# Kernel optimization log

Hardware: AMD Instinct MI355X
Metric: run time of the kernel (lower is better)

Reference implementation:

```python
import jax, jax.numpy as jnp
import numpy as np

N = 50000
E = 800000
D_IN = 128
D_H = 128
D_OUT = 128
G = 64
EPS = 1e-5


def setup_inputs() -> dict:
    key = jax.random.key(0)
    ks = jax.random.split(key, 16)
    s = 0.05
    x = jax.random.normal(ks[0], (N, D_IN), dtype=jnp.float32)
    edge_index = jax.random.randint(ks[1], (2, E), 0, N, dtype=jnp.int64)
    batch = jnp.sort(jax.random.randint(ks[2], (N,), 0, G, dtype=jnp.int64))
    return {
        "x": x,
        "edge_index": edge_index,
        "batch": batch,
        "W1": jax.random.normal(ks[3], (D_IN, D_H), jnp.float32) * s,
        "a_src1": jax.random.normal(ks[4], (D_H,), jnp.float32) * s,
        "a_dst1": jax.random.normal(ks[5], (D_H,), jnp.float32) * s,
        "b1": jnp.zeros((D_H,), jnp.float32),
        "W2": jax.random.normal(ks[6], (D_H, D_H), jnp.float32) * s,
        "a_src2": jax.random.normal(ks[7], (D_H,), jnp.float32) * s,
        "a_dst2": jax.random.normal(ks[8], (D_H,), jnp.float32) * s,
        "b2": jnp.zeros((D_H,), jnp.float32),
        "ln1_g": jnp.ones((D_H,), jnp.float32),
        "ln1_b": jnp.zeros((D_H,), jnp.float32),
        "ln2_g": jnp.ones((D_H,), jnp.float32),
        "ln2_b": jnp.zeros((D_H,), jnp.float32),
        "fc_W": jax.random.normal(ks[9], (D_H, D_OUT), jnp.float32) * s,
        "fc_b": jnp.zeros((D_OUT,), jnp.float32),
        "bn_g": jnp.ones((D_OUT,), jnp.float32),
        "bn_b": jnp.zeros((D_OUT,), jnp.float32),
    }


def gat_conv(x, src, dst, W, a_src, a_dst, b):
    # PyG GATConv, heads=1, concat=False. src=j (message source), dst=i (target).
    h = x @ W                              # [N, C]
    al_s = h @ a_src                       # [N]
    al_d = h @ a_dst                       # [N]
    alpha = jax.nn.leaky_relu(al_s[src] + al_d[dst], 0.2)  # [E']
    m = jax.ops.segment_max(alpha, dst, num_segments=N)    # segment softmax (stable)
    e = jnp.exp(alpha - m[dst])
    z = jax.ops.segment_sum(e, dst, num_segments=N)
    w = e / z[dst]                          # [E']
    out = jax.ops.segment_sum(w[:, None] * h[src], dst, num_segments=N)
    return out + b


def layer_norm(x, g, b):
    mu = jnp.mean(x, axis=-1, keepdims=True)
    var = jnp.mean((x - mu) ** 2, axis=-1, keepdims=True)
    return (x - mu) * jax.lax.rsqrt(var + EPS) * g + b


def reference(x, edge_index, batch, W1, a_src1, a_dst1, b1, W2, a_src2, a_dst2, b2,
              ln1_g, ln1_b, ln2_g, ln2_b, fc_W, fc_b, bn_g, bn_b):
    # add self loops (PyG GATConv default)
    sl = jnp.arange(N, dtype=edge_index.dtype)
    src = jnp.concatenate([edge_index[0], sl])
    dst = jnp.concatenate([edge_index[1], sl])

    h = jax.nn.relu(gat_conv(x, src, dst, W1, a_src1, a_dst1, b1))
    h = layer_norm(h, ln1_g, ln1_b)
    # dropout is identity in eval
    h = gat_conv(h, src, dst, W2, a_src2, a_dst2, b2)
    h = layer_norm(h, ln2_g, ln2_b)
    h = jax.nn.relu(h)

    # global mean pool over graphs
    sums = jax.ops.segment_sum(h, batch, num_segments=G)            # [G, D_H]
    cnts = jax.ops.segment_sum(jnp.ones((N,), h.dtype), batch, num_segments=G)
    pooled = sums / jnp.maximum(cnts, 1.0)[:, None]

    logits = pooled @ fc_W + fc_b                                   # [G, D_OUT]
    # BatchNorm1d (training-mode batch stats, biased variance)
    mu = jnp.mean(logits, axis=0)
    var = jnp.mean((logits - mu) ** 2, axis=0)
    logits = (logits - mu) * jax.lax.rsqrt(var + EPS) * bn_g + bn_b
    return logits
```

## Files before the change

kernel.cpp:

```cpp
#include <hip/hip_runtime.h>
#include <hip/hip_bf16.h>
#include <math.h>

#define N_NODES 50000
#define N_EDGES 800000
#define EN (N_EDGES + N_NODES)
#define D 128
#define G_GRAPHS 64
#define EPS 1e-5f
#define POOL_ROWS_PER_WAVE 64
#define N_TILES 3125

#define NBUCK 196
#define BCAP 8192
#define EPB 4096
#define BIN_BLOCKS ((EN + EPB - 1) / EPB)

typedef short short8 __attribute__((ext_vector_type(8)));
typedef float f32x4  __attribute__((ext_vector_type(4)));
typedef unsigned short us8 __attribute__((ext_vector_type(8)));

__device__ __forceinline__ float wave_reduce_sum(float v) {
  #pragma unroll
  for (int off = 32; off > 0; off >>= 1) v += __shfl_xor(v, off, 64);
  return v;
}
__device__ __forceinline__ int wave_reduce_sum_i(int v) {
  #pragma unroll
  for (int off = 32; off > 0; off >>= 1) v += __shfl_xor(v, off, 64);
  return v;
}

__device__ __forceinline__ float bf_to_f(unsigned short u) {
  union { unsigned int i; float f; } a;
  a.i = ((unsigned int)u) << 16;
  return a.f;
}
__device__ __forceinline__ unsigned short f_to_bf(float f) {
  union { float f; unsigned int i; } v; v.f = f;
  unsigned int r = v.i + 0x7FFF + ((v.i >> 16) & 1);
  return (unsigned short)(r >> 16);
}


__global__ __launch_bounds__(256) void bin_kernel(
    const int* __restrict__ ei, int* __restrict__ gcnt, uint2* __restrict__ bedges) {
  __shared__ int hist[NBUCK], base[NBUCK], curl[NBUCK];
  int tid = threadIdx.x;
  for (int i = tid; i < NBUCK; i += 256) { hist[i] = 0; curl[i] = 0; }
  __syncthreads();
  int e0 = blockIdx.x * EPB;
  int srcs[16], dsts[16];
  #pragma unroll
  for (int i = 0; i < 16; ++i) {
    int e = e0 + i * 256 + tid;
    int s = -1, d = -1;
    if (e < N_EDGES)   { s = ei[e]; d = ei[N_EDGES + e]; }
    else if (e < EN)   { s = e - N_EDGES; d = s; }
    srcs[i] = s; dsts[i] = d;
    if (d >= 0) atomicAdd(&hist[d >> 8], 1);
  }
  __syncthreads();
  for (int i = tid; i < NBUCK; i += 256)
    base[i] = atomicAdd(&gcnt[i], hist[i]);
  __syncthreads();
  #pragma unroll
  for (int i = 0; i < 16; ++i) {
    int d = dsts[i];
    if (d < 0) continue;
    int b = d >> 8;
    int pos = base[b] + atomicAdd(&curl[b], 1);
    if (pos < BCAP) bedges[(size_t)b * BCAP + pos] = make_uint2((unsigned)srcs[i], (unsigned)d);
  }
}

__global__ __launch_bounds__(256) void bucket_csr_kernel(
    const uint2* __restrict__ bedges, const int* __restrict__ gcnt,
    int* __restrict__ offs, int* __restrict__ esrc, float* __restrict__ sums) {
  __shared__ int hist[256], pex[256], curl[256], scanbuf[256];
  __shared__ int wsum[4];
  int b = blockIdx.x, t = threadIdx.x;
  if (b == 0) {
    for (int i = t; i < G_GRAPHS * D; i += 256) sums[i] = 0.f;
    if (t == 0) offs[N_NODES] = EN;
  }
  int pv = (t < b) ? gcnt[t] : 0;
  int v = wave_reduce_sum_i(pv);
  if ((t & 63) == 0) wsum[t >> 6] = v;
  hist[t] = 0; curl[t] = 0;
  __syncthreads();
  int gb = wsum[0] + wsum[1] + wsum[2] + wsum[3];
  int m = gcnt[b]; if (m > BCAP) m = BCAP;
  int node0 = b << 8;
  const uint2* be = bedges + (size_t)b * BCAP;
  for (int k = t; k < m; k += 256) atomicAdd(&hist[be[k].y & 255], 1);
  __syncthreads();
  int h = hist[t];
  scanbuf[t] = h;
  __syncthreads();
  #pragma unroll
  for (int off = 1; off < 256; off <<= 1) {
    int add = (t >= off) ? scanbuf[t - off] : 0;
    __syncthreads();
    scanbuf[t] += add;
    __syncthreads();
  }
  pex[t] = scanbuf[t] - h;
  int node = node0 + t;
  if (node < N_NODES) offs[node] = gb + pex[t];
  __syncthreads();
  for (int k = t; k < m; k += 256) {
    uint2 e = be[k];
    int n = e.y & 255;
    int r = atomicAdd(&curl[n], 1);
    esrc[gb + pex[n] + r] = (int)e.x;
  }
}


__global__ __launch_bounds__(256) void linear_mfma_kernel(
    const unsigned short* __restrict__ Xb, const float* __restrict__ Xf,
    const float* __restrict__ W,
    const float* __restrict__ a_s, const float* __restrict__ a_d,
    unsigned short* __restrict__ Hb, float* __restrict__ AS, float* __restrict__ AD) {
  __shared__ unsigned short Wl[D * D];
  int tid = threadIdx.x;
  #pragma unroll
  for (int it = 0; it < 64; ++it) {
    int flat = it * 256 + tid;
    int r = flat >> 7, col = flat & 127;
    int c = r >> 5, rem = r & 31, quad = rem >> 3, j = rem & 7;
    int t = col >> 4, l = quad * 16 + (col & 15);
    Wl[((t * 4 + c) * 64 + l) * 8 + j] = f_to_bf(W[flat]);
  }
  int lane = tid & 63, wv = tid >> 6;
  int colI = lane & 15, quad = lane >> 4;
  float as_v[8], ad_v[8];
  #pragma unroll
  for (int t = 0; t < 8; ++t) { as_v[t] = a_s[t * 16 + colI]; ad_v[t] = a_d[t * 16 + colI]; }
  __syncthreads();
  for (int tile = blockIdx.x * 4 + wv; tile < N_TILES; tile += gridDim.x * 4) {
    int row0 = tile * 16;
    short8 afr[4];
    if (Xf) {
      const float* xpf = Xf + (size_t)(row0 + colI) * D + quad * 8;
      #pragma unroll
      for (int c = 0; c < 4; ++c) {
        float4 f0 = *(const float4*)(xpf + c * 32);
        float4 f1 = *(const float4*)(xpf + c * 32 + 4);
        short8 a;
        a[0] = (short)f_to_bf(f0.x); a[1] = (short)f_to_bf(f0.y);
        a[2] = (short)f_to_bf(f0.z); a[3] = (short)f_to_bf(f0.w);
        a[4] = (short)f_to_bf(f1.x); a[5] = (short)f_to_bf(f1.y);
        a[6] = (short)f_to_bf(f1.z); a[7] = (short)f_to_bf(f1.w);
        afr[c] = a;
      }
    } else {
      const unsigned short* xp = Xb + (size_t)(row0 + colI) * D + quad * 8;
      #pragma unroll
      for (int c = 0; c < 4; ++c) afr[c] = *(const short8*)(xp + c * 32);
    }
    f32x4 acc[8];
    #pragma unroll
    for (int t = 0; t < 8; ++t) acc[t] = (f32x4){0.f, 0.f, 0.f, 0.f};
    #pragma unroll
    for (int t = 0; t < 8; ++t) {
      #pragma unroll
      for (int c = 0; c < 4; ++c) {
        short8 bfr = *(const short8*)&Wl[((t * 4 + c) * 64 + lane) * 8];
        acc[t] = __builtin_amdgcn_mfma_f32_16x16x32_bf16(afr[c], bfr, acc[t], 0, 0, 0);
      }
    }
    #pragma unroll
    for (int r = 0; r < 4; ++r) {
      int row = row0 + quad * 4 + r;
      float s = 0.f, dd = 0.f;
      #pragma unroll
      for (int t = 0; t < 8; ++t) {
        float v = acc[t][r];
        Hb[(size_t)row * D + t * 16 + colI] = f_to_bf(v);
        s  = fmaf(v, as_v[t], s);
        dd = fmaf(v, ad_v[t], dd);
      }
      #pragma unroll
      for (int off = 8; off >= 1; off >>= 1) {
        s  += __shfl_xor(s, off, 64);
        dd += __shfl_xor(dd, off, 64);
      }
      if (colI == 0) { AS[row] = s; AD[row] = dd; }
    }
  }
}


__global__ __launch_bounds__(256) void gat_kernel(
    const unsigned short* __restrict__ Hf, const float* __restrict__ AS,
    const float* __restrict__ AD,
    const int* __restrict__ offs, const int* __restrict__ esrc,
    const float* __restrict__ bias, const float* __restrict__ lng, const float* __restrict__ lnb,
    unsigned short* __restrict__ Out, int relu_after) {
  int tid = threadIdx.x;
  int lane = tid & 63;
  int wv = tid >> 6;
  int g4 = lane >> 4, mm = lane & 15;
  int node = blockIdx.x * 16 + wv * 4 + g4;
  if (node >= N_NODES) return;
  int beg = offs[node], end = offs[node + 1];
  float ald = AD[node];
  int base = lane & 48;
  float acc[8];
  #pragma unroll
  for (int d = 0; d < 8; ++d) acc[d] = 0.f;
  float zl = 0.f;
  const unsigned short* hq = Hf + 8 * mm;

  for (int c0 = beg; c0 < end; c0 += 16) {
    int nk = end - c0; if (nk > 16) nk = 16;
    int s_l = 0; float w_l = 0.f;
    if (mm < nk) {
      s_l = esrc[c0 + mm];
      float a = AS[s_l] + ald;
      a = (a > 0.f) ? a : 0.2f * a;
      w_l = __expf(a);
    }
    zl += w_l;
    int   sA = __shfl(s_l, base, 64),     sB = __shfl(s_l, base + 1, 64);
    float wA = __shfl(w_l, base, 64),     wB = __shfl(w_l, base + 1, 64);
    us8 hA = *(const us8*)(hq + (unsigned)sA * D);
    us8 hB = *(const us8*)(hq + (unsigned)sB * D);
    for (int j = 2; j < nk; j += 2) {
      int   sA1 = __shfl(s_l, base + j, 64),     sB1 = __shfl(s_l, base + j + 1, 64);
      float wA1 = __shfl(w_l, base + j, 64),     wB1 = __shfl(w_l, base + j + 1, 64);
      us8 hA1 = *(const us8*)(hq + (unsigned)sA1 * D);
      us8 hB1 = *(const us8*)(hq + (unsigned)sB1 * D);
      #pragma unroll
      for (int d = 0; d < 8; ++d) acc[d] = fmaf(wA, bf_to_f(hA[d]), acc[d]);
      #pragma unroll
      for (int d = 0; d < 8; ++d) acc[d] = fmaf(wB, bf_to_f(hB[d]), acc[d]);
      wA = wA1; wB = wB1; hA = hA1; hB = hB1;
    }
    #pragma unroll
    for (int d = 0; d < 8; ++d) acc[d] = fmaf(wA, bf_to_f(hA[d]), acc[d]);
    #pragma unroll
    for (int d = 0; d < 8; ++d) acc[d] = fmaf(wB, bf_to_f(hB[d]), acc[d]);
  }

  #pragma unroll
  for (int off = 8; off >= 1; off >>= 1) zl += __shfl_xor(zl, off, 64);
  float inv_z = 1.f / zl;
  const float4* bp = (const float4*)&bias[8 * mm];
  float4 bA4 = bp[0], bB4 = bp[1];
  float bb[8] = {bA4.x, bA4.y, bA4.z, bA4.w, bB4.x, bB4.y, bB4.z, bB4.w};
  float vv[8];
  #pragma unroll
  for (int d = 0; d < 8; ++d) {
    vv[d] = acc[d] * inv_z + bb[d];
    if (!relu_after) vv[d] = fmaxf(vv[d], 0.f);
  }
  float s8 = 0.f, ss = 0.f;
  #pragma unroll
  for (int d = 0; d < 8; ++d) { s8 += vv[d]; ss += vv[d] * vv[d]; }
  #pragma unroll
  for (int off = 8; off >= 1; off >>= 1) {
    s8 += __shfl_xor(s8, off, 64);
    ss += __shfl_xor(ss, off, 64);
  }
  float mean = s8 * (1.f / 128.f);
  float var = ss * (1.f / 128.f) - mean * mean;
  float inv = rsqrtf(var + EPS);
  const float4* gp = (const float4*)&lng[8 * mm];
  const float4* lp = (const float4*)&lnb[8 * mm];
  float4 gA = gp[0], gB = gp[1], lA = lp[0], lB = lp[1];
  float gg[8] = {gA.x, gA.y, gA.z, gA.w, gB.x, gB.y, gB.z, gB.w};
  float ll[8] = {lA.x, lA.y, lA.z, lA.w, lB.x, lB.y, lB.z, lB.w};
  us8 o;
  #pragma unroll
  for (int d = 0; d < 8; ++d) {
    float od = (vv[d] - mean) * inv * gg[d] + ll[d];
    if (relu_after) od = fmaxf(od, 0.f);
    o[d] = f_to_bf(od);
  }
  *(us8*)&Out[(size_t)node * D + 8 * mm] = o;
}


__global__ __launch_bounds__(256) void pool_sum_kernel(
    const unsigned short* __restrict__ Hf, const int* __restrict__ bat,
    float* __restrict__ sums) {
  int lane = threadIdx.x & 63;
  int g4 = lane >> 4, mm = lane & 15;
  int wv = blockIdx.x * 4 + (threadIdx.x >> 6);
  int r0 = wv * POOL_ROWS_PER_WAVE;
  if (r0 >= N_NODES) return;
  int r1 = r0 + POOL_ROWS_PER_WAVE;
  if (r1 > N_NODES) r1 = N_NODES;
  int rs = r0 + g4;
  if (rs >= r1) return;
  float acc[8];
  #pragma unroll
  for (int d = 0; d < 8; ++d) acc[d] = 0.f;
  int g = bat[rs];
  for (int r = rs; r < r1; r += 4) {
    int gr = bat[r];
    if (gr != g) {
      #pragma unroll
      for (int d = 0; d < 8; ++d) atomicAdd(&sums[g * D + 8 * mm + d], acc[d]);
      #pragma unroll
      for (int d = 0; d < 8; ++d) acc[d] = 0.f;
      g = gr;
    }
    us8 hv = *(const us8*)&Hf[(size_t)r * D + 8 * mm];
    #pragma unroll
    for (int d = 0; d < 8; ++d) acc[d] += bf_to_f(hv[d]);
  }
  #pragma unroll
  for (int d = 0; d < 8; ++d) atomicAdd(&sums[g * D + 8 * mm + d], acc[d]);
}

__device__ __forceinline__ int lower_bound_batch(const int* __restrict__ b, int val) {
  int lo = 0, hi = N_NODES;
  while (lo < hi) {
    int mid = (lo + hi) >> 1;
    if (b[mid] < val) lo = mid + 1; else hi = mid;
  }
  return lo;
}

__global__ void fc_kernel(const float* __restrict__ sums, const int* __restrict__ bat,
                          const float* __restrict__ fcW, const float* __restrict__ fcb,
                          float* __restrict__ logits) {
  int g = blockIdx.x;
  int d = threadIdx.x;
  int start = lower_bound_batch(bat, g);
  int end   = lower_bound_batch(bat, g + 1);
  float cnt = (float)(end - start);
  __shared__ float ps[D];
  ps[d] = sums[g * D + d] / fmaxf(cnt, 1.f);
  __syncthreads();
  float o = fcb[d];
  #pragma unroll 8
  for (int k = 0; k < D; ++k) o = fmaf(ps[k], fcW[k * D + d], o);
  logits[g * D + d] = o;
}

__global__ void bn_kernel(const float* __restrict__ logits, const float* __restrict__ g,
                          const float* __restrict__ b, float* __restrict__ out) {
  int d = threadIdx.x;
  float mu = 0.f;
  for (int i = 0; i < G_GRAPHS; ++i) mu += logits[i * D + d];
  mu *= (1.f / G_GRAPHS);
  float var = 0.f;
  for (int i = 0; i < G_GRAPHS; ++i) { float t = logits[i * D + d] - mu; var += t * t; }
  var *= (1.f / G_GRAPHS);
  float inv = rsqrtf(var + EPS);
  float gg = g[d], bb = b[d];
  for (int i = 0; i < G_GRAPHS; ++i)
    out[i * D + d] = (logits[i * D + d] - mu) * inv * gg + bb;
}


extern "C" void kernel_launch(void* const* d_in, const int* in_sizes, int n_in,
                              void* d_out, int out_size, void* d_ws, size_t ws_size,
                              hipStream_t stream) {
  const float* x    = (const float*)d_in[0];
  const int*   ei   = (const int*)d_in[1];
  const int*   bat  = (const int*)d_in[2];
  const float* W1   = (const float*)d_in[3];
  const float* as1  = (const float*)d_in[4];
  const float* ad1  = (const float*)d_in[5];
  const float* b1   = (const float*)d_in[6];
  const float* W2   = (const float*)d_in[7];
  const float* as2  = (const float*)d_in[8];
  const float* ad2  = (const float*)d_in[9];
  const float* b2   = (const float*)d_in[10];
  const float* ln1g = (const float*)d_in[11];
  const float* ln1b = (const float*)d_in[12];
  const float* ln2g = (const float*)d_in[13];
  const float* ln2b = (const float*)d_in[14];
  const float* fcW  = (const float*)d_in[15];
  const float* fcb  = (const float*)d_in[16];
  const float* bng  = (const float*)d_in[17];
  const float* bnb  = (const float*)d_in[18];

  char* p = (char*)d_ws;
  auto carve = [&](size_t bytes) { char* r = p; p += (bytes + 255) & ~(size_t)255; return r; };
  int*   offs  = (int*)carve((N_NODES + 1) * sizeof(int));
  int*   gcnt  = (int*)carve(NBUCK * sizeof(int));
  int*   esrc  = (int*)carve((size_t)EN * sizeof(int));
  float* AS    = (float*)carve(N_NODES * sizeof(float));
  float* AD    = (float*)carve(N_NODES * sizeof(float));
  float* LG    = (float*)carve((size_t)G_GRAPHS * D * sizeof(float));
  float* SUMS  = (float*)carve((size_t)G_GRAPHS * D * sizeof(float));
  unsigned short* B1b = (unsigned short*)carve((size_t)N_NODES * D * sizeof(unsigned short));
  unsigned short* B2b = (unsigned short*)carve((size_t)N_NODES * D * sizeof(unsigned short));
  uint2* bedges = (uint2*)B1b;

  const int RB = (N_NODES + 15) / 16;
  const int PB = (N_NODES + 4 * POOL_ROWS_PER_WAVE - 1) / (4 * POOL_ROWS_PER_WAVE);
  const int LB = 256;

  hipMemsetAsync(gcnt, 0, NBUCK * sizeof(int), stream);
  bin_kernel<<<BIN_BLOCKS, 256, 0, stream>>>(ei, gcnt, bedges);
  bucket_csr_kernel<<<NBUCK, 256, 0, stream>>>(bedges, gcnt, offs, esrc, SUMS);

  linear_mfma_kernel<<<LB, 256, 0, stream>>>(nullptr, x, W1, as1, ad1, B1b, AS, AD);
  gat_kernel<<<RB, 256, 0, stream>>>(B1b, AS, AD, offs, esrc, b1, ln1g, ln1b, B2b, 0);
  linear_mfma_kernel<<<LB, 256, 0, stream>>>(B2b, nullptr, W2, as2, ad2, B1b, AS, AD);
  gat_kernel<<<RB, 256, 0, stream>>>(B1b, AS, AD, offs, esrc, b2, ln2g, ln2b, B2b, 1);

  pool_sum_kernel<<<PB, 256, 0, stream>>>(B2b, bat, SUMS);
  fc_kernel<<<G_GRAPHS, D, 0, stream>>>(SUMS, bat, fcW, fcb, LG);
  bn_kernel<<<1, D, 0, stream>>>(LG, bng, bnb, (float*)d_out);
}
```

Measured before the change: 255.7 us.

## Fuse mean-pool into second GAT kernel and merge FC with BatchNorm

The second GAT layer now accumulates its LayerNorm+ReLU output directly into per-graph sums through shared-memory atomics, flushed to global atomics. This removes the bf16 write of the final node features and the separate pool_sum pass. The FC and BatchNorm kernels are merged into one single-block kernel, and the inner FMA uses packed 2-wide float vectors with cheaper bf16 unpacking. The fused FC kernel is a single block with a 128-entry register array per thread, which may serialize. Dropping the node>=N guard relies on N being divisible by 16.

Result: slower. 268.9 us (+5.2%).

```diff
diff --git a/kernel.cpp b/kernel.cpp
--- a/kernel.cpp
+++ b/kernel.cpp
@@ -8,7 +8,6 @@
 #define D 128
 #define G_GRAPHS 64
 #define EPS 1e-5f
-#define POOL_ROWS_PER_WAVE 64
 #define N_TILES 3125
 
 #define NBUCK 196
@@ -19,18 +18,13 @@
 typedef short short8 __attribute__((ext_vector_type(8)));
 typedef float f32x4  __attribute__((ext_vector_type(4)));
 typedef unsigned short us8 __attribute__((ext_vector_type(8)));
-
-__device__ __forceinline__ float wave_reduce_sum(float v) {
+typedef float v2f __attribute__((ext_vector_type(2)));
+
+__device__ __forceinline__ int wave_reduce_sum_i(int v) {
   #pragma unroll
   for (int off = 32; off > 0; off >>= 1) v += __shfl_xor(v, off, 64);
   return v;
 }
-__device__ __forceinline__ int wave_reduce_sum_i(int v) {
-  #pragma unroll
-  for (int off = 32; off > 0; off >>= 1) v += __shfl_xor(v, off, 64);
-  return v;
-}
-
 __device__ __forceinline__ float bf_to_f(unsigned short u) {
   union { unsigned int i; float f; } a;
   a.i = ((unsigned int)u) << 16;
@@ -40,6 +34,18 @@
   union { float f; unsigned int i; } v; v.f = f;
   unsigned int r = v.i + 0x7FFF + ((v.i >> 16) & 1);
   return (unsigned short)(r >> 16);
+}
+__device__ __forceinline__ float u_as_f(unsigned int u) {
+  union { unsigned int i; float f; } a; a.i = u; return a.f;
+}
+__device__ __forceinline__ void acc_row(v2f acc2[4], const unsigned short* rp, float w) {
+  uint4 uv = *(const uint4*)rp;
+  v2f wv; wv.x = w; wv.y = w;
+  v2f h;
+  h.x = u_as_f(uv.x << 16); h.y = u_as_f(uv.x & 0xFFFF0000u); acc2[0] += wv * h;
+  h.x = u_as_f(uv.y << 16); h.y = u_as_f(uv.y & 0xFFFF0000u); acc2[1] += wv * h;
+  h.x = u_as_f(uv.z << 16); h.y = u_as_f(uv.z & 0xFFFF0000u); acc2[2] += wv * h;
+  h.x = u_as_f(uv.w << 16); h.y = u_as_f(uv.w & 0xFFFF0000u); acc2[3] += wv * h;
 }
 
 
@@ -198,19 +204,22 @@
     const float* __restrict__ AD,
     const int* __restrict__ offs, const int* __restrict__ esrc,
     const float* __restrict__ bias, const float* __restrict__ lng, const float* __restrict__ lnb,
-    unsigned short* __restrict__ Out, int relu_after) {
+    unsigned short* __restrict__ Out, const int* __restrict__ bat,
+    float* __restrict__ sums, int mode) {
+  __shared__ float gsum[4][D];
   int tid = threadIdx.x;
+  for (int i = tid; i < 4 * D; i += 256) ((float*)gsum)[i] = 0.f;
+  __syncthreads();
   int lane = tid & 63;
   int wv = tid >> 6;
   int g4 = lane >> 4, mm = lane & 15;
   int node = blockIdx.x * 16 + wv * 4 + g4;
-  if (node >= N_NODES) return;
   int beg = offs[node], end = offs[node + 1];
   float ald = AD[node];
   int base = lane & 48;
-  float acc[8];
-  #pragma unroll
-  for (int d = 0; d < 8; ++d) acc[d] = 0.f;
+  v2f acc2[4];
+  #pragma unroll
+  for (int i = 0; i < 4; ++i) { acc2[i].x = 0.f; acc2[i].y = 0.f; }
   float zl = 0.f;
   const unsigned short* hq = Hf + 8 * mm;
 
@@ -233,16 +242,12 @@
       float wA1 = __shfl(w_l, base + j, 64),     wB1 = __shfl(w_l, base + j + 1, 64);
       us8 hA1 = *(const us8*)(hq + (unsigned)sA1 * D);
       us8 hB1 = *(const us8*)(hq + (unsigned)sB1 * D);
-      #pragma unroll
-      for (int d = 0; d < 8; ++d) acc[d] = fmaf(wA, bf_to_f(hA[d]), acc[d]);
-      #pragma unroll
-      for (int d = 0; d < 8; ++d) acc[d] = fmaf(wB, bf_to_f(hB[d]), acc[d]);
+      acc_row(acc2, (const unsigned short*)&hA, wA);
+      acc_row(acc2, (const unsigned short*)&hB, wB);
       wA = wA1; wB = wB1; hA = hA1; hB = hB1;
     }
-    #pragma unroll
-    for (int d = 0; d < 8; ++d) acc[d] = fmaf(wA, bf_to_f(hA[d]), acc[d]);
-    #pragma unroll
-    for (int d = 0; d < 8; ++d) acc[d] = fmaf(wB, bf_to_f(hB[d]), acc[d]);
+    acc_row(acc2, (const unsigned short*)&hA, wA);
+    acc_row(acc2, (const unsigned short*)&hB, wB);
   }
 
   #pragma unroll
@@ -253,9 +258,11 @@
   float bb[8] = {bA4.x, bA4.y, bA4.z, bA4.w, bB4.x, bB4.y, bB4.z, bB4.w};
   float vv[8];
   #pragma unroll
+  for (int i = 0; i < 4; ++i) { vv[2*i] = acc2[i].x; vv[2*i+1] = acc2[i].y; }
+  #pragma unroll
   for (int d = 0; d < 8; ++d) {
-    vv[d] = acc[d] * inv_z + bb[d];
-    if (!relu_after) vv[d] = fmaxf(vv[d], 0.f);
+    vv[d] = vv[d] * inv_z + bb[d];
+    if (mode == 0) vv[d] = fmaxf(vv[d], 0.f);
   }
   float s8 = 0.f, ss = 0.f;
   #pragma unroll
@@ -273,89 +280,88 @@
   float4 gA = gp[0], gB = gp[1], lA = lp[0], lB = lp[1];
   float gg[8] = {gA.x, gA.y, gA.z, gA.w, gB.x, gB.y, gB.z, gB.w};
   float ll[8] = {lA.x, lA.y, lA.z, lA.w, lB.x, lB.y, lB.z, lB.w};
-  us8 o;
+  float od[8];
   #pragma unroll
   for (int d = 0; d < 8; ++d) {
-    float od = (vv[d] - mean) * inv * gg[d] + ll[d];
-    if (relu_after) od = fmaxf(od, 0.f);
-    o[d] = f_to_bf(od);
-  }
-  *(us8*)&Out[(size_t)node * D + 8 * mm] = o;
-}
-
-
-__global__ __launch_bounds__(256) void pool_sum_kernel(
-    const unsigned short* __restrict__ Hf, const int* __restrict__ bat,
-    float* __restrict__ sums) {
-  int lane = threadIdx.x & 63;
-  int g4 = lane >> 4, mm = lane & 15;
-  int wv = blockIdx.x * 4 + (threadIdx.x >> 6);
-  int r0 = wv * POOL_ROWS_PER_WAVE;
-  if (r0 >= N_NODES) return;
-  int r1 = r0 + POOL_ROWS_PER_WAVE;
-  if (r1 > N_NODES) r1 = N_NODES;
-  int rs = r0 + g4;
-  if (rs >= r1) return;
-  float acc[8];
-  #pragma unroll
-  for (int d = 0; d < 8; ++d) acc[d] = 0.f;
-  int g = bat[rs];
-  for (int r = rs; r < r1; r += 4) {
-    int gr = bat[r];
-    if (gr != g) {
-      #pragma unroll
-      for (int d = 0; d < 8; ++d) atomicAdd(&sums[g * D + 8 * mm + d], acc[d]);
-      #pragma unroll
-      for (int d = 0; d < 8; ++d) acc[d] = 0.f;
-      g = gr;
-    }
-    us8 hv = *(const us8*)&Hf[(size_t)r * D + 8 * mm];
+    od[d] = (vv[d] - mean) * inv * gg[d] + ll[d];
+    if (mode == 1) od[d] = fmaxf(od[d], 0.f);
+  }
+
+  if (mode == 0) {
+    us8 o;
     #pragma unroll
-    for (int d = 0; d < 8; ++d) acc[d] += bf_to_f(hv[d]);
-  }
-  #pragma unroll
-  for (int d = 0; d < 8; ++d) atomicAdd(&sums[g * D + 8 * mm + d], acc[d]);
-}
-
-__device__ __forceinline__ int lower_bound_batch(const int* __restrict__ b, int val) {
-  int lo = 0, hi = N_NODES;
-  while (lo < hi) {
-    int mid = (lo + hi) >> 1;
-    if (b[mid] < val) lo = mid + 1; else hi = mid;
-  }
-  return lo;
-}
-
-__global__ void fc_kernel(const float* __restrict__ sums, const int* __restrict__ bat,
-                          const float* __restrict__ fcW, const float* __restrict__ fcb,
-                          float* __restrict__ logits) {
-  int g = blockIdx.x;
-  int d = threadIdx.x;
-  int start = lower_bound_batch(bat, g);
-  int end   = lower_bound_batch(bat, g + 1);
-  float cnt = (float)(end - start);
-  __shared__ float ps[D];
-  ps[d] = sums[g * D + d] / fmaxf(cnt, 1.f);
-  __syncthreads();
-  float o = fcb[d];
-  #pragma unroll 8
-  for (int k = 0; k < D; ++k) o = fmaf(ps[k], fcW[k * D + d], o);
-  logits[g * D + d] = o;
-}
-
-__global__ void bn_kernel(const float* __restrict__ logits, const float* __restrict__ g,
-                          const float* __restrict__ b, float* __restrict__ out) {
-  int d = threadIdx.x;
-  float mu = 0.f;
-  for (int i = 0; i < G_GRAPHS; ++i) mu += logits[i * D + d];
-  mu *= (1.f / G_GRAPHS);
-  float var = 0.f;
-  for (int i = 0; i < G_GRAPHS; ++i) { float t = logits[i * D + d] - mu; var += t * t; }
-  var *= (1.f / G_GRAPHS);
+    for (int d = 0; d < 8; ++d) o[d] = f_to_bf(od[d]);
+    *(us8*)&Out[(size_t)node * D + 8 * mm] = o;
+  } else {
+    int g0 = bat[blockIdx.x * 16];
+    int gl = bat[node] - g0;
+    if (gl < 4) {
+      #pragma unroll
+      for (int d = 0; d < 8; ++d) atomicAdd(&gsum[gl][8 * mm + d], od[d]);
+    } else {
+      #pragma unroll
+      for (int d = 0; d < 8; ++d) atomicAdd(&sums[(g0 + gl) * D + 8 * mm + d], od[d]);
+    }
+  }
+  __syncthreads();
+  if (mode == 1) {
+    int g0 = bat[blockIdx.x * 16];
+    for (int i = tid; i < 4 * D; i += 256) {
+      float v = ((float*)gsum)[i];
+      int j = i >> 7;
+      if (v != 0.f && g0 + j < G_GRAPHS)
+        atomicAdd(&sums[(g0 + j) * D + (i & 127)], v);
+    }
+  }
+}
+
+
+__global__ __launch_bounds__(256) void fc_bn_kernel(
+    const float* __restrict__ sums, const int* __restrict__ bat,
+    const float* __restrict__ fcW, const float* __restrict__ fcb,
+    const float* __restrict__ bng, const float* __restrict__ bnb,
+    float* __restrict__ out) {
+  __shared__ float ps[G_GRAPHS * D];
+  __shared__ int starts[G_GRAPHS + 1];
+  __shared__ float red[2][2][D];
+  int t = threadIdx.x;
+  if (t <= G_GRAPHS) {
+    int lo = 0, hi = N_NODES;
+    while (lo < hi) { int mid = (lo + hi) >> 1; if (bat[mid] < t) lo = mid + 1; else hi = mid; }
+    starts[t] = lo;
+  }
+  __syncthreads();
+  for (int i = t; i < G_GRAPHS * D; i += 256) {
+    int g = i >> 7;
+    float cnt = (float)(starts[g + 1] - starts[g]);
+    ps[i] = sums[i] / fmaxf(cnt, 1.f);
+  }
+  __syncthreads();
+  int d = t & 127, gh = t >> 7;
+  float wcol[D];
+  #pragma unroll
+  for (int k = 0; k < D; ++k) wcol[k] = fcW[k * D + d];
+  float fb = fcb[d];
+  float lg[32];
+  float m = 0.f, sq = 0.f;
+  for (int j = 0; j < 32; ++j) {
+    int g = gh * 32 + j;
+    float acc = fb;
+    #pragma unroll
+    for (int k = 0; k < D; ++k) acc = fmaf(ps[g * D + k], wcol[k], acc);
+    lg[j] = acc;
+    m += acc; sq += acc * acc;
+  }
+  red[gh][0][d] = m; red[gh][1][d] = sq;
+  __syncthreads();
+  float mu = (red[0][0][d] + red[1][0][d]) * (1.f / G_GRAPHS);
+  float var = (red[0][1][d] + red[1][1][d]) * (1.f / G_GRAPHS) - mu * mu;
   float inv = rsqrtf(var + EPS);
-  float gg = g[d], bb = b[d];
-  for (int i = 0; i < G_GRAPHS; ++i)
-    out[i * D + d] = (logits[i * D + d] - mu) * inv * gg + bb;
+  float gg = bng[d], bb = bnb[d];
+  for (int j = 0; j < 32; ++j) {
+    int g = gh * 32 + j;
+    out[g * D + d] = (lg[j] - mu) * inv * gg + bb;
+  }
 }
 
 
@@ -389,14 +395,12 @@
   int*   esrc  = (int*)carve((size_t)EN * sizeof(int));
   float* AS    = (float*)carve(N_NODES * sizeof(float));
   float* AD    = (float*)carve(N_NODES * sizeof(float));
-  float* LG    = (float*)carve((size_t)G_GRAPHS * D * sizeof(float));
   float* SUMS  = (float*)carve((size_t)G_GRAPHS * D * sizeof(float));
   unsigned short* B1b = (unsigned short*)carve((size_t)N_NODES * D * sizeof(unsigned short));
   unsigned short* B2b = (unsigned short*)carve((size_t)N_NODES * D * sizeof(unsigned short));
   uint2* bedges = (uint2*)B1b;
 
   const int RB = (N_NODES + 15) / 16;
-  const int PB = (N_NODES + 4 * POOL_ROWS_PER_WAVE - 1) / (4 * POOL_ROWS_PER_WAVE);
   const int LB = 256;
 
   hipMemsetAsync(gcnt, 0, NBUCK * sizeof(int), stream);
@@ -404,11 +408,11 @@
   bucket_csr_kernel<<<NBUCK, 256, 0, stream>>>(bedges, gcnt, offs, esrc, SUMS);
 
   linear_mfma_kernel<<<LB, 256, 0, stream>>>(nullptr, x, W1, as1, ad1, B1b, AS, AD);
-  gat_kernel<<<RB, 256, 0, stream>>>(B1b, AS, AD, offs, esrc, b1, ln1g, ln1b, B2b, 0);
+  gat_kernel<<<RB, 256, 0, stream>>>(B1b, AS, AD, offs, esrc, b1, ln1g, ln1b,
+                                     B2b, bat, SUMS, 0);
   linear_mfma_kernel<<<LB, 256, 0, stream>>>(B2b, nullptr, W2, as2, ad2, B1b, AS, AD);
-  gat_kernel<<<RB, 256, 0, stream>>>(B1b, AS, AD, offs, esrc, b2, ln2g, ln2b, B2b, 1);
-
-  pool_sum_kernel<<<PB, 256, 0, stream>>>(B2b, bat, SUMS);
-  fc_kernel<<<G_GRAPHS, D, 0, stream>>>(SUMS, bat, fcW, fcb, LG);
-  bn_kernel<<<1, D, 0, stream>>>(LG, bng, bnb, (float*)d_out);
-}
+  gat_kernel<<<RB, 256, 0, stream>>>(B1b, AS, AD, offs, esrc, b2, ln2g, ln2b,
+                                     nullptr, bat, SUMS, 1);
+
+  fc_bn_kernel<<<1, 256, 0, stream>>>(SUMS, bat, fcW, fcb, bng, bnb, (float*)d_out);
+}
```
